# Kernel tuning notes

Hardware: AMD Instinct MI355X
Metric: run time of the kernel (lower is better)

Reference implementation:

```python
import jax, jax.numpy as jnp
import numpy as np

EPS = 1e-8


def setup_inputs() -> dict:
    key = jax.random.key(0)
    k1, k2, k3, k4 = jax.random.split(key, 4)
    N, D, P, H = 8192, 512, 128, 128
    x1 = jax.random.normal(k1, (N, D), dtype=jnp.float32)
    proj_w1 = jax.random.normal(k2, (D, D), dtype=jnp.float32) * (1.0 / np.sqrt(D))
    proj_w2 = jax.random.normal(k3, (D, P), dtype=jnp.float32) * (1.0 / np.sqrt(D))
    gc_w = jax.random.normal(k4, (D, H), dtype=jnp.float32) * (1.0 / np.sqrt(D))
    gc_b = jnp.zeros((H,), dtype=jnp.float32)
    return {"x1": x1, "proj_w1": proj_w1, "proj_w2": proj_w2, "gc_w": gc_w, "gc_b": gc_b}


def _cosine_similarity(x):
    # torch.mm(x, x.T) / clamp(||x|| * ||x||.T, eps)
    w = jnp.sqrt(jnp.sum(x * x, axis=1, keepdims=True))  # [N,1]
    return (x @ x.T) / jnp.maximum(w * w.T, EPS)


def reference(x1, proj_w1, proj_w2, gc_w, gc_b):
    # projector: Linear(512,512,bias=False) -> ReLU -> Linear(512,P,bias=False)
    x_proj = jax.nn.relu(x1 @ proj_w1) @ proj_w2  # [N,P]
    # graph build is under @torch.no_grad(): dense fully-connected weighted graph
    A = jax.lax.stop_gradient(_cosine_similarity(x_proj))  # [N,N]
    N = x1.shape[0]
    # WGraphConv (DGL GraphConv w/ edge weights, norm='both'):
    # fully connected graph incl. self loops -> in_degree = N, norm = N^{-1/2} on both sides
    inv_n = jnp.asarray(1.0 / N, dtype=x1.dtype)
    h = x1 @ gc_w            # project first (D > H, cheaper)  [N,H]
    h = (A @ h) * inv_n      # weighted aggregate, symmetric degree norm
    return h + gc_b          # [N,H]
```

## Files before the change

### kernel.cpp

```cpp
#include <hip/hip_runtime.h>
#include <stdint.h>
#include <stddef.h>

typedef short s16x4 __attribute__((ext_vector_type(4)));
typedef short s16x8 __attribute__((ext_vector_type(8)));
typedef float f32x4 __attribute__((ext_vector_type(4)));

#define NN 8192
#define DD 512
#define PP 128
#define HH 128

__device__ __forceinline__ short f2bf(float f) {
  unsigned u = __builtin_bit_cast(unsigned, f);
  u = (u + 0x7fffu + ((u >> 16) & 1u)) >> 16;
  return (short)u;
}

__device__ __forceinline__ void async16(const void* g, void* l) {
  __builtin_amdgcn_global_load_lds(
      (const __attribute__((address_space(1))) unsigned int*)g,
      (__attribute__((address_space(3))) unsigned int*)l, 16, 0, 0);
}

template <int MF>
__device__ __forceinline__ void gemm_core2(
    const short* __restrict__ A, long lda,
    const short* __restrict__ BT, long ldb,
    long rowBase, long colBase, int k0, int k1,
    short* As0, short* Bs0, short* As1, short* Bs1,
    f32x4 (*acc)[4]) {
  const int tid  = threadIdx.x;
  const int lane = tid & 63;
  const int wid  = tid >> 6;
  const int wr   = (wid >> 1) * (MF * 16);
  const int wc   = (wid & 1) * 64;
  const int srow = lane >> 3;
  const int skk  = (lane & 7) * 8;

#define STAGE_(AS, BS, KK)                                                    \
  do {                                                                        \
    _Pragma("unroll")                                                         \
    for (int it = 0; it < MF; ++it) {                                         \
      int r = wid * (MF * 8) + it * 8;                                        \
      async16(A + (rowBase + r + srow) * lda + (KK) + skk, (AS) + r * 64);    \
    }                                                                         \
    _Pragma("unroll")                                                         \
    for (int it = 0; it < 4; ++it) {                                          \
      int r = wid * 32 + it * 8;                                              \
      async16(BT + (colBase + r + srow) * ldb + (KK) + skk, (BS) + r * 64);   \
    }                                                                         \
  } while (0)

  STAGE_(As0, Bs0, k0);
  __syncthreads();
  for (int k = k0; k < k1; k += 64) {
    if (k + 64 < k1) STAGE_(As1, Bs1, k + 64);
#pragma unroll
    for (int ks = 0; ks < 64; ks += 32) {
      s16x8 af[MF], bfv[4];
#pragma unroll
      for (int i = 0; i < MF; ++i)
        af[i]  = *(const s16x8*)(As0 + (wr + i * 16 + (lane & 15)) * 64 + ks + (lane >> 4) * 8);
#pragma unroll
      for (int i = 0; i < 4; ++i)
        bfv[i] = *(const s16x8*)(Bs0 + (wc + i * 16 + (lane & 15)) * 64 + ks + (lane >> 4) * 8);
#pragma unroll
      for (int mi = 0; mi < MF; ++mi)
#pragma unroll
        for (int ni = 0; ni < 4; ++ni)
          acc[mi][ni] = __builtin_amdgcn_mfma_f32_16x16x32_bf16(af[mi], bfv[ni], acc[mi][ni], 0, 0, 0);
    }
    __syncthreads();
    short* t0 = As0; As0 = As1; As1 = t0;
    short* t1 = Bs0; Bs0 = Bs1; Bs1 = t1;
  }
#undef STAGE_
}

__device__ __forceinline__ void zero_acc2(f32x4 (*acc)[4], int mf) {
  f32x4 z = {0.f, 0.f, 0.f, 0.f};
  for (int i = 0; i < mf; ++i)
    for (int j = 0; j < 4; ++j) acc[i][j] = z;
}

__global__ __launch_bounds__(256) void k_prep(
    const float* __restrict__ x1, const float* __restrict__ w1,
    const float* __restrict__ w2, const float* __restrict__ gcw,
    short* __restrict__ x1b, short* __restrict__ w1t,
    short* __restrict__ w2t, short* __restrict__ gcwt) {
  long b = blockIdx.x;
  int t = threadIdx.x;
  if (b < 4096) {
    long i = b * 256 + t;
    float4 v = ((const float4*)x1)[i];
    s16x4 o;
    o[0] = f2bf(v.x); o[1] = f2bf(v.y); o[2] = f2bf(v.z); o[3] = f2bf(v.w);
    *(s16x4*)(x1b + i * 4) = o;
  } else if (b < 4096 + 1024) {
    long i = (b - 4096) * 256 + t;
    int n = (int)(i >> 9), k = (int)(i & 511);
    w1t[i] = f2bf(w1[(long)k * DD + n]);
  } else if (b < 4096 + 1024 + 256) {
    long i = (b - 5120) * 256 + t;
    int n = (int)(i >> 9), k = (int)(i & 511);
    w2t[i] = f2bf(w2[(long)k * PP + n]);
  } else {
    long i = (b - 5376) * 256 + t;
    int n = (int)(i >> 9), k = (int)(i & 511);
    gcwt[i] = f2bf(gcw[(long)k * HH + n]);
  }
}

__global__ __launch_bounds__(256) void k_g13(const short* __restrict__ x1b,
                                             const short* __restrict__ w1t,
                                             const short* __restrict__ gcwt,
                                             short* __restrict__ Y,
                                             short* __restrict__ hT) {
  __shared__ __align__(16) char smem[49152];
  short* As0 = (short*)smem;
  short* As1 = (short*)(smem + 8192);
  short* Bs0 = (short*)(smem + 16384);
  short* Bs1 = (short*)(smem + 32768);
  f32x4 acc[2][4];
  zero_acc2(acc, 2);
  const int bx = blockIdx.x;
  const int lane = threadIdx.x & 63, wid = threadIdx.x >> 6;
  const int wr = (wid >> 1) * 32, wc = (wid & 1) * 64;
  if (bx < 512) {
    long rowBase = (long)(bx >> 2) * 64;
    long colBase = (long)(bx & 3) * 128;
    gemm_core2<2>(x1b, DD, w1t, DD, rowBase, colBase, 0, DD, As0, Bs0, As1, Bs1, acc);
#pragma unroll
    for (int mi = 0; mi < 2; ++mi)
#pragma unroll
      for (int ni = 0; ni < 4; ++ni)
#pragma unroll
        for (int r = 0; r < 4; ++r) {
          long m = rowBase + wr + mi * 16 + ((lane >> 4) << 2) + r;
          long n = colBase + wc + ni * 16 + (lane & 15);
          float v = acc[mi][ni][r];
          Y[m * DD + n] = f2bf(v > 0.f ? v : 0.f);
        }
  } else {
    long rowBase = (long)(bx - 512) * 64;
    gemm_core2<2>(x1b, DD, gcwt, DD, rowBase, 0, 0, DD, As0, Bs0, As1, Bs1, acc);
    short (*hs)[66] = (short(*)[66])smem;
#pragma unroll
    for (int mi = 0; mi < 2; ++mi)
#pragma unroll
      for (int ni = 0; ni < 4; ++ni)
#pragma unroll
        for (int r = 0; r < 4; ++r) {
          int m = wr + mi * 16 + ((lane >> 4) << 2) + r;
          int n = wc + ni * 16 + (lane & 15);
          hs[n][m] = f2bf(acc[mi][ni][r]);
        }
    __syncthreads();
    int t = threadIdx.x;
    int h = t >> 1, m0 = (t & 1) * 32;
#pragma unroll
    for (int j0 = 0; j0 < 32; j0 += 8) {
      s16x8 o;
#pragma unroll
      for (int u = 0; u < 8; ++u) o[u] = hs[h][m0 + j0 + u];
      *(s16x8*)(hT + (long)h * NN + rowBase + m0 + j0) = o;
    }
  }
}

__global__ __launch_bounds__(256) void k_g2e(const short* __restrict__ Y,
                                             const short* __restrict__ w2t,
                                             const short* __restrict__ hT,
                                             short* __restrict__ xp,
                                             float* __restrict__ invnw,
                                             float* __restrict__ Gp) {
  __shared__ __align__(16) char smem[50176];
  short* As0 = (short*)smem;
  short* As1 = (short*)(smem + 8192);
  short* Bs0 = (short*)(smem + 16384);
  short* Bs1 = (short*)(smem + 32768);
  f32x4 acc[2][4];
  zero_acc2(acc, 2);
  const long rowBase = (long)blockIdx.x * 64;
  gemm_core2<2>(Y, DD, w2t, DD, rowBase, 0, 0, DD, As0, Bs0, As1, Bs1, acc);
  const int t = threadIdx.x;
  const int lane = t & 63, wid = t >> 6;
  {
    const int wr = (wid >> 1) * 32, wc = (wid & 1) * 64;
    float (*xs)[129] = (float(*)[129])smem;
    float* invw_s = (float*)(smem + 49920);
    short* xpt_s = (short*)(smem + 33536);
#pragma unroll
    for (int mi = 0; mi < 2; ++mi)
#pragma unroll
      for (int ni = 0; ni < 4; ++ni)
#pragma unroll
        for (int r = 0; r < 4; ++r)
          xs[wr + mi * 16 + ((lane >> 4) << 2) + r][wc + ni * 16 + (lane & 15)] = acc[mi][ni][r];
    __syncthreads();
    if (t < 64) {
      float s = 0.f;
#pragma unroll 8
      for (int i = 0; i < 128; ++i) { int c = (t + i) & 127; float v = xs[t][c]; s += v * v; }
      float nr = sqrtf(s);
      invnw[rowBase + t] = 1.f / (8192.f * nr);
      invw_s[t] = 1.f / nr;
    }
    __syncthreads();
#pragma unroll
    for (int i = 0; i < 4; ++i) {
      int seg = i * 256 + t;
      int r = seg >> 4, c0 = (seg & 15) * 8;
      s16x8 o;
#pragma unroll
      for (int u = 0; u < 8; ++u) o[u] = f2bf(xs[r][c0 + u]);
      *(s16x8*)(xp + (long)(rowBase + r) * PP + c0) = o;
    }
    int c = t >> 1, n0 = (t & 1) * 32;
#pragma unroll
    for (int j0 = 0; j0 < 32; j0 += 8) {
      s16x8 o;
#pragma unroll
      for (int u = 0; u < 8; ++u) {
        int n = n0 + j0 + u;
        o[u] = f2bf(xs[n][c] * invw_s[n]);
      }
      *(s16x8*)(xpt_s + c * 64 + n0 + j0) = o;
    }
  }
  __syncthreads();
  {
    short* hts = (short*)smem;
    const int srow = lane >> 3, skk = (lane & 7) * 8;
#pragma unroll
    for (int it = 0; it < 4; ++it) {
      int r = wid * 32 + it * 8;
      async16(hT + (long)(r + srow) * NN + rowBase + skk, hts + r * 64);
    }
  }
  __syncthreads();
  {
    const short* xpt_s = (const short*)(smem + 33536);
    const short* hts = (const short*)smem;
    const int wr = (wid >> 1) * 64, wc = (wid & 1) * 64;
    f32x4 acc2[4][4];
    zero_acc2(acc2, 4);
#pragma unroll
    for (int ks = 0; ks < 64; ks += 32) {
      s16x8 af[4], bfv[4];
#pragma unroll
      for (int i = 0; i < 4; ++i)
        af[i]  = *(const s16x8*)(xpt_s + (wr + i * 16 + (lane & 15)) * 64 + ks + (lane >> 4) * 8);
#pragma unroll
      for (int i = 0; i < 4; ++i)
        bfv[i] = *(const s16x8*)(hts + (wc + i * 16 + (lane & 15)) * 64 + ks + (lane >> 4) * 8);
#pragma unroll
      for (int mi = 0; mi < 4; ++mi)
#pragma unroll
        for (int ni = 0; ni < 4; ++ni)
          acc2[mi][ni] = __builtin_amdgcn_mfma_f32_16x16x32_bf16(af[mi], bfv[ni], acc2[mi][ni], 0, 0, 0);
    }
    float* gp = Gp + (long)blockIdx.x * (PP * HH);
#pragma unroll
    for (int mi = 0; mi < 4; ++mi)
#pragma unroll
      for (int ni = 0; ni < 4; ++ni)
#pragma unroll
        for (int r = 0; r < 4; ++r) {
          int m = wr + mi * 16 + ((lane >> 4) << 2) + r;
          int n = wc + ni * 16 + (lane & 15);
          gp[m * HH + n] = acc2[mi][ni][r];
        }
  }
}

__global__ __launch_bounds__(256) void k_red(const float* __restrict__ Gp,
                                             short* __restrict__ GT) {
  int i = blockIdx.x * 256 + threadIdx.x;
  float s = 0.f;
#pragma unroll 8
  for (int j = 0; j < 128; ++j) s += Gp[j * (PP * HH) + i];
  int p = i >> 7, h = i & 127;
  GT[h * PP + p] = f2bf(s);
}

__global__ __launch_bounds__(256) void k_gf(const short* __restrict__ xp,
                                            const short* __restrict__ GT,
                                            const float* __restrict__ invnw,
                                            const float* __restrict__ gcb,
                                            float* __restrict__ out) {
  __shared__ __align__(16) char smem[49152];
  short* As0 = (short*)smem;
  short* As1 = (short*)(smem + 8192);
  short* Bs0 = (short*)(smem + 16384);
  short* Bs1 = (short*)(smem + 32768);
  f32x4 acc[2][4];
  zero_acc2(acc, 2);
  long rowBase = (long)blockIdx.x * 64;
  gemm_core2<2>(xp, PP, GT, PP, rowBase, 0, 0, PP, As0, Bs0, As1, Bs1, acc);
  const int lane = threadIdx.x & 63, wid = threadIdx.x >> 6;
  const int wr = (wid >> 1) * 32, wc = (wid & 1) * 64;
#pragma unroll
  for (int mi = 0; mi < 2; ++mi)
#pragma unroll
    for (int ni = 0; ni < 4; ++ni)
#pragma unroll
      for (int r = 0; r < 4; ++r) {
        long m = rowBase + wr + mi * 16 + ((lane >> 4) << 2) + r;
        int n = wc + ni * 16 + (lane & 15);
        out[m * HH + n] = acc[mi][ni][r] * invnw[m] + gcb[n];
      }
}

extern "C" void kernel_launch(void* const* d_in, const int* in_sizes, int n_in,
                              void* d_out, int out_size, void* d_ws, size_t ws_size,
                              hipStream_t stream) {
  const float* x1  = (const float*)d_in[0];
  const float* w1  = (const float*)d_in[1];
  const float* w2  = (const float*)d_in[2];
  const float* gcw = (const float*)d_in[3];
  const float* gcb = (const float*)d_in[4];
  float* out = (float*)d_out;

  char* ws = (char*)d_ws;
  size_t off = 0;
  auto alloc = [&](size_t bytes) -> char* {
    char* p = ws + off;
    off += (bytes + 255) & ~(size_t)255;
    return p;
  };
  short* x1b  = (short*)alloc((size_t)NN * DD * 2);
  short* w1t  = (short*)alloc((size_t)DD * DD * 2);
  short* w2t  = (short*)alloc((size_t)PP * DD * 2);
  short* gcwt = (short*)alloc((size_t)HH * DD * 2);
  short* Y    = (short*)alloc((size_t)NN * DD * 2);
  short* xp   = (short*)alloc((size_t)NN * PP * 2);
  short* hT   = (short*)alloc((size_t)NN * HH * 2);
  float* invnw = (float*)alloc((size_t)NN * 4);
  float* Gp   = (float*)alloc((size_t)128 * PP * HH * 4);
  short* GT   = (short*)alloc((size_t)PP * HH * 2);

  hipLaunchKernelGGL(k_prep, dim3(5632), dim3(256), 0, stream,
                     x1, w1, w2, gcw, x1b, w1t, w2t, gcwt);
  hipLaunchKernelGGL(k_g13, dim3(640), dim3(256), 0, stream, x1b, w1t, gcwt, Y, hT);
  hipLaunchKernelGGL(k_g2e, dim3(128), dim3(256), 0, stream, Y, w2t, hT, xp, invnw, Gp);
  hipLaunchKernelGGL(k_red, dim3(64), dim3(256), 0, stream, Gp, GT);
  hipLaunchKernelGGL(k_gf, dim3(128), dim3(256), 0, stream, xp, GT, invnw, gcb, out);
}
```

Baseline: 49.94 us.

## Fuse tail kernels into one persistent kernel with atomic grid barriers

Merges the projection/partial-Gram kernel, the reduction kernel and the final GEMM kernel into a single 128-block kernel separated by software grid barriers built on atomic counters. The aim is to remove two kernel launch boundaries and their drain/ramp gaps on a small tail workload. A memset of the counters is added each call. The barrier relies on all 128 blocks being co-resident, and during the reduction only half the threads work.

```diff
diff --git a/kernel.cpp b/kernel.cpp
--- a/kernel.cpp
+++ b/kernel.cpp
@@ -21,6 +21,17 @@
   __builtin_amdgcn_global_load_lds(
       (const __attribute__((address_space(1))) unsigned int*)g,
       (__attribute__((address_space(3))) unsigned int*)l, 16, 0, 0);
+}
+
+__device__ __forceinline__ void gridbar(unsigned* cnt, unsigned expected) {
+  __threadfence();
+  __syncthreads();
+  if (threadIdx.x == 0) {
+    atomicAdd(cnt, 1u);
+    while (atomicAdd(cnt, 0u) < expected) __builtin_amdgcn_s_sleep(2);
+  }
+  __syncthreads();
+  __threadfence();
 }
 
 template <int MF>
@@ -169,148 +180,151 @@
   }
 }
 
-__global__ __launch_bounds__(256) void k_g2e(const short* __restrict__ Y,
-                                             const short* __restrict__ w2t,
-                                             const short* __restrict__ hT,
-                                             short* __restrict__ xp,
-                                             float* __restrict__ invnw,
-                                             float* __restrict__ Gp) {
+__global__ __launch_bounds__(256) void k_tail(const short* __restrict__ Y,
+                                              const short* __restrict__ w2t,
+                                              const short* __restrict__ hT,
+                                              const float* __restrict__ gcb,
+                                              short* __restrict__ xp,
+                                              float* __restrict__ invnw,
+                                              float* __restrict__ Gp,
+                                              short* __restrict__ GT,
+                                              float* __restrict__ out,
+                                              unsigned* __restrict__ cnt) {
   __shared__ __align__(16) char smem[50176];
-  short* As0 = (short*)smem;
-  short* As1 = (short*)(smem + 8192);
-  short* Bs0 = (short*)(smem + 16384);
-  short* Bs1 = (short*)(smem + 32768);
-  f32x4 acc[2][4];
-  zero_acc2(acc, 2);
-  const long rowBase = (long)blockIdx.x * 64;
-  gemm_core2<2>(Y, DD, w2t, DD, rowBase, 0, 0, DD, As0, Bs0, As1, Bs1, acc);
   const int t = threadIdx.x;
   const int lane = t & 63, wid = t >> 6;
+  const long rowBase = (long)blockIdx.x * 64;
+
   {
+    short* As0 = (short*)smem;
+    short* As1 = (short*)(smem + 8192);
+    short* Bs0 = (short*)(smem + 16384);
+    short* Bs1 = (short*)(smem + 32768);
+    f32x4 acc[2][4];
+    zero_acc2(acc, 2);
+    gemm_core2<2>(Y, DD, w2t, DD, rowBase, 0, 0, DD, As0, Bs0, As1, Bs1, acc);
+    {
+      const int wr = (wid >> 1) * 32, wc = (wid & 1) * 64;
+      float (*xs)[129] = (float(*)[129])smem;
+      float* invw_s = (float*)(smem + 49920);
+      short* xpt_s = (short*)(smem + 33536);
+#pragma unroll
+      for (int mi = 0; mi < 2; ++mi)
+#pragma unroll
+        for (int ni = 0; ni < 4; ++ni)
+#pragma unroll
+          for (int r = 0; r < 4; ++r)
+            xs[wr + mi * 16 + ((lane >> 4) << 2) + r][wc + ni * 16 + (lane & 15)] = acc[mi][ni][r];
+      __syncthreads();
+      if (t < 64) {
+        float s = 0.f;
+#pragma unroll 8
+        for (int i = 0; i < 128; ++i) { int c = (t + i) & 127; float v = xs[t][c]; s += v * v; }
+        float nr = sqrtf(s);
+        invnw[rowBase + t] = 1.f / (8192.f * nr);
+        invw_s[t] = 1.f / nr;
+      }
+      __syncthreads();
+#pragma unroll
+      for (int i = 0; i < 4; ++i) {
+        int seg = i * 256 + t;
+        int r = seg >> 4, c0 = (seg & 15) * 8;
+        s16x8 o;
+#pragma unroll
+        for (int u = 0; u < 8; ++u) o[u] = f2bf(xs[r][c0 + u]);
+        *(s16x8*)(xp + (long)(rowBase + r) * PP + c0) = o;
+      }
+      int c = t >> 1, n0 = (t & 1) * 32;
+#pragma unroll
+      for (int j0 = 0; j0 < 32; j0 += 8) {
+        s16x8 o;
+#pragma unroll
+        for (int u = 0; u < 8; ++u) {
+          int n = n0 + j0 + u;
+          o[u] = f2bf(xs[n][c] * invw_s[n]);
+        }
+        *(s16x8*)(xpt_s + c * 64 + n0 + j0) = o;
+      }
+    }
+    __syncthreads();
+    {
+      short* hts = (short*)smem;
+      const int srow = lane >> 3, skk = (lane & 7) * 8;
+#pragma unroll
+      for (int it = 0; it < 4; ++it) {
+        int r = wid * 32 + it * 8;
+        async16(hT + (long)(r + srow) * NN + rowBase + skk, hts + r * 64);
+      }
+    }
+    __syncthreads();
+    {
+      const short* xpt_s = (const short*)(smem + 33536);
+      const short* hts = (const short*)smem;
+      const int wr = (wid >> 1) * 64, wc = (wid & 1) * 64;
+      f32x4 acc2[4][4];
+      zero_acc2(acc2, 4);
+#pragma unroll
+      for (int ks = 0; ks < 64; ks += 32) {
+        s16x8 af[4], bfv[4];
+#pragma unroll
+        for (int i = 0; i < 4; ++i)
+          af[i]  = *(const s16x8*)(xpt_s + (wr + i * 16 + (lane & 15)) * 64 + ks + (lane >> 4) * 8);
+#pragma unroll
+        for (int i = 0; i < 4; ++i)
+          bfv[i] = *(const s16x8*)(hts + (wc + i * 16 + (lane & 15)) * 64 + ks + (lane >> 4) * 8);
+#pragma unroll
+        for (int mi = 0; mi < 4; ++mi)
+#pragma unroll
+          for (int ni = 0; ni < 4; ++ni)
+            acc2[mi][ni] = __builtin_amdgcn_mfma_f32_16x16x32_bf16(af[mi], bfv[ni], acc2[mi][ni], 0, 0, 0);
+      }
+      float* gp = Gp + (long)blockIdx.x * (PP * HH);
+#pragma unroll
+      for (int mi = 0; mi < 4; ++mi)
+#pragma unroll
+        for (int ni = 0; ni < 4; ++ni)
+#pragma unroll
+          for (int r = 0; r < 4; ++r) {
+            int m = wr + mi * 16 + ((lane >> 4) << 2) + r;
+            int n = wc + ni * 16 + (lane & 15);
+            gp[m * HH + n] = acc2[mi][ni][r];
+          }
+    }
+  }
+
+  gridbar(cnt, 128);
+
+  if (t < 128) {
+    int i = blockIdx.x * 128 + t;
+    float s = 0.f;
+#pragma unroll 8
+    for (int j = 0; j < 128; ++j) s += Gp[j * (PP * HH) + i];
+    int p = i >> 7, h = i & 127;
+    GT[h * PP + p] = f2bf(s);
+  }
+
+  gridbar(cnt + 1, 128);
+
+  {
+    short* As0 = (short*)smem;
+    short* As1 = (short*)(smem + 8192);
+    short* Bs0 = (short*)(smem + 16384);
+    short* Bs1 = (short*)(smem + 32768);
+    f32x4 acc[2][4];
+    zero_acc2(acc, 2);
+    gemm_core2<2>(xp, PP, GT, PP, rowBase, 0, 0, PP, As0, Bs0, As1, Bs1, acc);
     const int wr = (wid >> 1) * 32, wc = (wid & 1) * 64;
-    float (*xs)[129] = (float(*)[129])smem;
-    float* invw_s = (float*)(smem + 49920);
-    short* xpt_s = (short*)(smem + 33536);
 #pragma unroll
     for (int mi = 0; mi < 2; ++mi)
 #pragma unroll
       for (int ni = 0; ni < 4; ++ni)
 #pragma unroll
-        for (int r = 0; r < 4; ++r)
-          xs[wr + mi * 16 + ((lane >> 4) << 2) + r][wc + ni * 16 + (lane & 15)] = acc[mi][ni][r];
-    __syncthreads();
-    if (t < 64) {
-      float s = 0.f;
-#pragma unroll 8
-      for (int i = 0; i < 128; ++i) { int c = (t + i) & 127; float v = xs[t][c]; s += v * v; }
-      float nr = sqrtf(s);
-      invnw[rowBase + t] = 1.f / (8192.f * nr);
-      invw_s[t] = 1.f / nr;
-    }
-    __syncthreads();
-#pragma unroll
-    for (int i = 0; i < 4; ++i) {
-      int seg = i * 256 + t;
-      int r = seg >> 4, c0 = (seg & 15) * 8;
-      s16x8 o;
-#pragma unroll
-      for (int u = 0; u < 8; ++u) o[u] = f2bf(xs[r][c0 + u]);
-      *(s16x8*)(xp + (long)(rowBase + r) * PP + c0) = o;
-    }
-    int c = t >> 1, n0 = (t & 1) * 32;
-#pragma unroll
-    for (int j0 = 0; j0 < 32; j0 += 8) {
-      s16x8 o;
-#pragma unroll
-      for (int u = 0; u < 8; ++u) {
-        int n = n0 + j0 + u;
-        o[u] = f2bf(xs[n][c] * invw_s[n]);
-      }
-      *(s16x8*)(xpt_s + c * 64 + n0 + j0) = o;
-    }
-  }
-  __syncthreads();
-  {
-    short* hts = (short*)smem;
-    const int srow = lane >> 3, skk = (lane & 7) * 8;
-#pragma unroll
-    for (int it = 0; it < 4; ++it) {
-      int r = wid * 32 + it * 8;
-      async16(hT + (long)(r + srow) * NN + rowBase + skk, hts + r * 64);
-    }
-  }
-  __syncthreads();
-  {
-    const short* xpt_s = (const short*)(smem + 33536);
-    const short* hts = (const short*)smem;
-    const int wr = (wid >> 1) * 64, wc = (wid & 1) * 64;
-    f32x4 acc2[4][4];
-    zero_acc2(acc2, 4);
-#pragma unroll
-    for (int ks = 0; ks < 64; ks += 32) {
-      s16x8 af[4], bfv[4];
-#pragma unroll
-      for (int i = 0; i < 4; ++i)
-        af[i]  = *(const s16x8*)(xpt_s + (wr + i * 16 + (lane & 15)) * 64 + ks + (lane >> 4) * 8);
-#pragma unroll
-      for (int i = 0; i < 4; ++i)
-        bfv[i] = *(const s16x8*)(hts + (wc + i * 16 + (lane & 15)) * 64 + ks + (lane >> 4) * 8);
-#pragma unroll
-      for (int mi = 0; mi < 4; ++mi)
-#pragma unroll
-        for (int ni = 0; ni < 4; ++ni)
-          acc2[mi][ni] = __builtin_amdgcn_mfma_f32_16x16x32_bf16(af[mi], bfv[ni], acc2[mi][ni], 0, 0, 0);
-    }
-    float* gp = Gp + (long)blockIdx.x * (PP * HH);
-#pragma unroll
-    for (int mi = 0; mi < 4; ++mi)
-#pragma unroll
-      for (int ni = 0; ni < 4; ++ni)
-#pragma unroll
         for (int r = 0; r < 4; ++r) {
-          int m = wr + mi * 16 + ((lane >> 4) << 2) + r;
+          long m = rowBase + wr + mi * 16 + ((lane >> 4) << 2) + r;
           int n = wc + ni * 16 + (lane & 15);
-          gp[m * HH + n] = acc2[mi][ni][r];
+          out[m * HH + n] = acc[mi][ni][r] * invnw[m] + gcb[n];
         }
   }
-}
-
-__global__ __launch_bounds__(256) void k_red(const float* __restrict__ Gp,
-                                             short* __restrict__ GT) {
-  int i = blockIdx.x * 256 + threadIdx.x;
-  float s = 0.f;
-#pragma unroll 8
-  for (int j = 0; j < 128; ++j) s += Gp[j * (PP * HH) + i];
-  int p = i >> 7, h = i & 127;
-  GT[h * PP + p] = f2bf(s);
-}
-
-__global__ __launch_bounds__(256) void k_gf(const short* __restrict__ xp,
-                                            const short* __restrict__ GT,
-                                            const float* __restrict__ invnw,
-                                            const float* __restrict__ gcb,
-                                            float* __restrict__ out) {
-  __shared__ __align__(16) char smem[49152];
-  short* As0 = (short*)smem;
-  short* As1 = (short*)(smem + 8192);
-  short* Bs0 = (short*)(smem + 16384);
-  short* Bs1 = (short*)(smem + 32768);
-  f32x4 acc[2][4];
-  zero_acc2(acc, 2);
-  long rowBase = (long)blockIdx.x * 64;
-  gemm_core2<2>(xp, PP, GT, PP, rowBase, 0, 0, PP, As0, Bs0, As1, Bs1, acc);
-  const int lane = threadIdx.x & 63, wid = threadIdx.x >> 6;
-  const int wr = (wid >> 1) * 32, wc = (wid & 1) * 64;
-#pragma unroll
-  for (int mi = 0; mi < 2; ++mi)
-#pragma unroll
-    for (int ni = 0; ni < 4; ++ni)
-#pragma unroll
-      for (int r = 0; r < 4; ++r) {
-        long m = rowBase + wr + mi * 16 + ((lane >> 4) << 2) + r;
-        int n = wc + ni * 16 + (lane & 15);
-        out[m * HH + n] = acc[mi][ni][r] * invnw[m] + gcb[n];
-      }
 }
 
 extern "C" void kernel_launch(void* const* d_in, const int* in_sizes, int n_in,
@@ -340,11 +354,12 @@
   float* invnw = (float*)alloc((size_t)NN * 4);
   float* Gp   = (float*)alloc((size_t)128 * PP * HH * 4);
   short* GT   = (short*)alloc((size_t)PP * HH * 2);
-
+  unsigned* cnt = (unsigned*)alloc(256);
+
+  hipMemsetAsync(cnt, 0, 8, stream);
   hipLaunchKernelGGL(k_prep, dim3(5632), dim3(256), 0, stream,
                      x1, w1, w2, gcw, x1b, w1t, w2t, gcwt);
   hipLaunchKernelGGL(k_g13, dim3(640), dim3(256), 0, stream, x1b, w1t, gcwt, Y, hT);
-  hipLaunchKernelGGL(k_g2e, dim3(128), dim3(256), 0, stream, Y, w2t, hT, xp, invnw, Gp);
-  hipLaunchKernelGGL(k_red, dim3(64), dim3(256), 0, stream, Gp, GT);
-  hipLaunchKernelGGL(k_gf, dim3(128), dim3(256), 0, stream, xp, GT, invnw, gcb, out);
-}
+  hipLaunchKernelGGL(k_tail, dim3(128), dim3(256), 0, stream,
+                     Y, w2t, hT, gcb, xp, invnw, Gp, GT, out, cnt);
+}
```

After: 101.3 us. 103% more time.

## Fuse x1 bf16 conversion into first GEMM and tile-transpose weight prep

Applied to the files above, without the earlier changes.

Removes the separate pass that converted x1 (16 MB fp32) to a bf16 copy. The first GEMM kernel now loads fp32 x1 directly into registers, converts it, and writes bf16 into LDS, with software prefetch of the next k-tile. Weight transposes now go through an LDS tile with coalesced reads and writes, and that kernel runs only 96 blocks. The cost is that x1 is reread as fp32 by every column block of the GEMM (4 for G1 plus 1 for the gc GEMM), which adds global traffic and register pressure.

```diff
diff --git a/kernel.cpp b/kernel.cpp
--- a/kernel.cpp
+++ b/kernel.cpp
@@ -84,35 +84,37 @@
     for (int j = 0; j < 4; ++j) acc[i][j] = z;
 }
 
-__global__ __launch_bounds__(256) void k_prep(
-    const float* __restrict__ x1, const float* __restrict__ w1,
-    const float* __restrict__ w2, const float* __restrict__ gcw,
-    short* __restrict__ x1b, short* __restrict__ w1t,
-    short* __restrict__ w2t, short* __restrict__ gcwt) {
-  long b = blockIdx.x;
-  int t = threadIdx.x;
-  if (b < 4096) {
-    long i = b * 256 + t;
-    float4 v = ((const float4*)x1)[i];
+__global__ __launch_bounds__(256) void k_prep_w(
+    const float* __restrict__ w1, const float* __restrict__ w2,
+    const float* __restrict__ gcw,
+    short* __restrict__ w1t, short* __restrict__ w2t, short* __restrict__ gcwt) {
+  __shared__ float tile[64][65];
+  int b = blockIdx.x, t = threadIdx.x;
+  const float* src; short* dst; int K0, N0, ldn;
+  if (b < 64)      { src = w1;  dst = w1t;  ldn = 512; K0 = (b >> 3) * 64;        N0 = (b & 7) * 64; }
+  else if (b < 80) { int bb = b - 64; src = w2;  dst = w2t;  ldn = 128; K0 = (bb >> 1) * 64; N0 = (bb & 1) * 64; }
+  else             { int bb = b - 80; src = gcw; dst = gcwt; ldn = 128; K0 = (bb >> 1) * 64; N0 = (bb & 1) * 64; }
+#pragma unroll
+  for (int i = 0; i < 4; ++i) {
+    int idx = i * 1024 + t * 4;
+    int row = idx >> 6, col = idx & 63;
+    float4 v = *(const float4*)(src + (long)(K0 + row) * ldn + N0 + col);
+    tile[row][col] = v.x; tile[row][col + 1] = v.y;
+    tile[row][col + 2] = v.z; tile[row][col + 3] = v.w;
+  }
+  __syncthreads();
+#pragma unroll
+  for (int i = 0; i < 4; ++i) {
+    int idx = i * 1024 + t * 4;
+    int n = idx >> 6, k = idx & 63;
     s16x4 o;
-    o[0] = f2bf(v.x); o[1] = f2bf(v.y); o[2] = f2bf(v.z); o[3] = f2bf(v.w);
-    *(s16x4*)(x1b + i * 4) = o;
-  } else if (b < 4096 + 1024) {
-    long i = (b - 4096) * 256 + t;
-    int n = (int)(i >> 9), k = (int)(i & 511);
-    w1t[i] = f2bf(w1[(long)k * DD + n]);
-  } else if (b < 4096 + 1024 + 256) {
-    long i = (b - 5120) * 256 + t;
-    int n = (int)(i >> 9), k = (int)(i & 511);
-    w2t[i] = f2bf(w2[(long)k * PP + n]);
-  } else {
-    long i = (b - 5376) * 256 + t;
-    int n = (int)(i >> 9), k = (int)(i & 511);
-    gcwt[i] = f2bf(gcw[(long)k * HH + n]);
-  }
-}
-
-__global__ __launch_bounds__(256) void k_g13(const short* __restrict__ x1b,
+#pragma unroll
+    for (int u = 0; u < 4; ++u) o[u] = f2bf(tile[k + u][n]);
+    *(s16x4*)(dst + (long)(N0 + n) * DD + K0 + k) = o;
+  }
+}
+
+__global__ __launch_bounds__(256) void k_g13(const float* __restrict__ x1,
                                              const short* __restrict__ w1t,
                                              const short* __restrict__ gcwt,
                                              short* __restrict__ Y,
@@ -124,13 +126,67 @@
   short* Bs1 = (short*)(smem + 32768);
   f32x4 acc[2][4];
   zero_acc2(acc, 2);
+  const int tid = threadIdx.x;
+  const int lane = tid & 63, wid = tid >> 6;
+  const int wr = (wid >> 1) * 32, wc = (wid & 1) * 64;
+  const int srow = lane >> 3, skk = (lane & 7) * 8;
+  const int arow = tid >> 2, ac0 = (tid & 3) * 16;
   const int bx = blockIdx.x;
-  const int lane = threadIdx.x & 63, wid = threadIdx.x >> 6;
-  const int wr = (wid >> 1) * 32, wc = (wid & 1) * 64;
-  if (bx < 512) {
-    long rowBase = (long)(bx >> 2) * 64;
-    long colBase = (long)(bx & 3) * 128;
-    gemm_core2<2>(x1b, DD, w1t, DD, rowBase, colBase, 0, DD, As0, Bs0, As1, Bs1, acc);
+  const bool isG1 = bx < 512;
+  const long rowBase = isG1 ? (long)(bx >> 2) * 64 : (long)(bx - 512) * 64;
+  const long colBase = isG1 ? (long)(bx & 3) * 128 : 0;
+  const short* BT = isG1 ? w1t : gcwt;
+  const float* aptr = x1 + (rowBase + arow) * DD + ac0;
+
+  float4 a0, a1, a2, a3;
+#define LOADA_(KK)                                                            \
+  do { const float4* p = (const float4*)(aptr + (KK));                        \
+       a0 = p[0]; a1 = p[1]; a2 = p[2]; a3 = p[3]; } while (0)
+#define LOADB_(BS, KK)                                                        \
+  do { _Pragma("unroll")                                                      \
+    for (int it = 0; it < 4; ++it) {                                          \
+      int r = wid * 32 + it * 8;                                              \
+      async16(BT + (colBase + r + srow) * DD + (KK) + skk, (BS) + r * 64);    \
+    } } while (0)
+#define WRITEA_(AS)                                                           \
+  do { s16x8 o0, o1;                                                          \
+    o0[0]=f2bf(a0.x); o0[1]=f2bf(a0.y); o0[2]=f2bf(a0.z); o0[3]=f2bf(a0.w);   \
+    o0[4]=f2bf(a1.x); o0[5]=f2bf(a1.y); o0[6]=f2bf(a1.z); o0[7]=f2bf(a1.w);   \
+    o1[0]=f2bf(a2.x); o1[1]=f2bf(a2.y); o1[2]=f2bf(a2.z); o1[3]=f2bf(a2.w);   \
+    o1[4]=f2bf(a3.x); o1[5]=f2bf(a3.y); o1[6]=f2bf(a3.z); o1[7]=f2bf(a3.w);   \
+    *(s16x8*)((AS) + arow * 64 + ac0)     = o0;                               \
+    *(s16x8*)((AS) + arow * 64 + ac0 + 8) = o1; } while (0)
+
+  LOADA_(0); LOADB_(Bs0, 0); WRITEA_(As0);
+  __syncthreads();
+  for (int k = 0; k < DD; k += 64) {
+    const bool more = (k + 64 < DD);
+    if (more) { LOADA_(k + 64); LOADB_(Bs1, k + 64); }
+#pragma unroll
+    for (int ks = 0; ks < 64; ks += 32) {
+      s16x8 af[2], bfv[4];
+#pragma unroll
+      for (int i = 0; i < 2; ++i)
+        af[i]  = *(const s16x8*)(As0 + (wr + i * 16 + (lane & 15)) * 64 + ks + (lane >> 4) * 8);
+#pragma unroll
+      for (int i = 0; i < 4; ++i)
+        bfv[i] = *(const s16x8*)(Bs0 + (wc + i * 16 + (lane & 15)) * 64 + ks + (lane >> 4) * 8);
+#pragma unroll
+      for (int mi = 0; mi < 2; ++mi)
+#pragma unroll
+        for (int ni = 0; ni < 4; ++ni)
+          acc[mi][ni] = __builtin_amdgcn_mfma_f32_16x16x32_bf16(af[mi], bfv[ni], acc[mi][ni], 0, 0, 0);
+    }
+    if (more) WRITEA_(As1);
+    __syncthreads();
+    short* t0 = As0; As0 = As1; As1 = t0;
+    short* t1 = Bs0; Bs0 = Bs1; Bs1 = t1;
+  }
+#undef LOADA_
+#undef LOADB_
+#undef WRITEA_
+
+  if (isG1) {
 #pragma unroll
     for (int mi = 0; mi < 2; ++mi)
 #pragma unroll
@@ -143,8 +199,6 @@
           Y[m * DD + n] = f2bf(v > 0.f ? v : 0.f);
         }
   } else {
-    long rowBase = (long)(bx - 512) * 64;
-    gemm_core2<2>(x1b, DD, gcwt, DD, rowBase, 0, 0, DD, As0, Bs0, As1, Bs1, acc);
     short (*hs)[66] = (short(*)[66])smem;
 #pragma unroll
     for (int mi = 0; mi < 2; ++mi)
@@ -157,8 +211,7 @@
           hs[n][m] = f2bf(acc[mi][ni][r]);
         }
     __syncthreads();
-    int t = threadIdx.x;
-    int h = t >> 1, m0 = (t & 1) * 32;
+    int h = tid >> 1, m0 = (tid & 1) * 32;
 #pragma unroll
     for (int j0 = 0; j0 < 32; j0 += 8) {
       s16x8 o;
@@ -330,7 +383,6 @@
     off += (bytes + 255) & ~(size_t)255;
     return p;
   };
-  short* x1b  = (short*)alloc((size_t)NN * DD * 2);
   short* w1t  = (short*)alloc((size_t)DD * DD * 2);
   short* w2t  = (short*)alloc((size_t)PP * DD * 2);
   short* gcwt = (short*)alloc((size_t)HH * DD * 2);
@@ -341,9 +393,8 @@
   float* Gp   = (float*)alloc((size_t)128 * PP * HH * 4);
   short* GT   = (short*)alloc((size_t)PP * HH * 2);
 
-  hipLaunchKernelGGL(k_prep, dim3(5632), dim3(256), 0, stream,
-                     x1, w1, w2, gcw, x1b, w1t, w2t, gcwt);
-  hipLaunchKernelGGL(k_g13, dim3(640), dim3(256), 0, stream, x1b, w1t, gcwt, Y, hT);
+  hipLaunchKernelGGL(k_prep_w, dim3(96), dim3(256), 0, stream, w1, w2, gcw, w1t, w2t, gcwt);
+  hipLaunchKernelGGL(k_g13, dim3(640), dim3(256), 0, stream, x1, w1t, gcwt, Y, hT);
   hipLaunchKernelGGL(k_g2e, dim3(128), dim3(256), 0, stream, Y, w2t, hT, xp, invnw, Gp);
   hipLaunchKernelGGL(k_red, dim3(64), dim3(256), 0, stream, Gp, GT);
   hipLaunchKernelGGL(k_gf, dim3(128), dim3(256), 0, stream, xp, GT, invnw, gcb, out);
```

Result: slower. 53.56 us (+7.2%).

## Halve row tiles in tail GEMMs and use LDS-tiled weight transposes

Applied to the files above, without the earlier changes.

The weight transpose-and-convert step now goes through a 64x64 shared-memory tile, so global reads and writes are coalesced instead of strided per-element. The projection/epilogue kernel and the final GEMM now process 32 rows per block instead of 64, doubling grid size to 256 blocks to fill more of the GPU's compute units. The partial Gram reduction sums 256 partials instead of 128. In exchange, per-block reuse drops and the reduction kernel reads twice as much partial data.

```diff
diff --git a/kernel.cpp b/kernel.cpp
--- a/kernel.cpp
+++ b/kernel.cpp
@@ -89,6 +89,7 @@
     const float* __restrict__ w2, const float* __restrict__ gcw,
     short* __restrict__ x1b, short* __restrict__ w1t,
     short* __restrict__ w2t, short* __restrict__ gcwt) {
+  __shared__ float tile[64][65];
   long b = blockIdx.x;
   int t = threadIdx.x;
   if (b < 4096) {
@@ -97,18 +98,30 @@
     s16x4 o;
     o[0] = f2bf(v.x); o[1] = f2bf(v.y); o[2] = f2bf(v.z); o[3] = f2bf(v.w);
     *(s16x4*)(x1b + i * 4) = o;
-  } else if (b < 4096 + 1024) {
-    long i = (b - 4096) * 256 + t;
-    int n = (int)(i >> 9), k = (int)(i & 511);
-    w1t[i] = f2bf(w1[(long)k * DD + n]);
-  } else if (b < 4096 + 1024 + 256) {
-    long i = (b - 5120) * 256 + t;
-    int n = (int)(i >> 9), k = (int)(i & 511);
-    w2t[i] = f2bf(w2[(long)k * PP + n]);
-  } else {
-    long i = (b - 5376) * 256 + t;
-    int n = (int)(i >> 9), k = (int)(i & 511);
-    gcwt[i] = f2bf(gcw[(long)k * HH + n]);
+    return;
+  }
+  int bb = (int)(b - 4096);
+  const float* src; short* dst; int K0, N0, ldn;
+  if (bb < 64)      { src = w1;  dst = w1t;  ldn = 512; K0 = (bb >> 3) * 64; N0 = (bb & 7) * 64; }
+  else if (bb < 80) { int c = bb - 64; src = w2;  dst = w2t;  ldn = 128; K0 = (c >> 1) * 64; N0 = (c & 1) * 64; }
+  else              { int c = bb - 80; src = gcw; dst = gcwt; ldn = 128; K0 = (c >> 1) * 64; N0 = (c & 1) * 64; }
+#pragma unroll
+  for (int i = 0; i < 4; ++i) {
+    int idx = i * 1024 + t * 4;
+    int row = idx >> 6, col = idx & 63;
+    float4 v = *(const float4*)(src + (long)(K0 + row) * ldn + N0 + col);
+    tile[row][col] = v.x; tile[row][col + 1] = v.y;
+    tile[row][col + 2] = v.z; tile[row][col + 3] = v.w;
+  }
+  __syncthreads();
+#pragma unroll
+  for (int i = 0; i < 4; ++i) {
+    int idx = i * 1024 + t * 4;
+    int n = idx >> 6, k = idx & 63;
+    s16x4 o;
+#pragma unroll
+    for (int u = 0; u < 4; ++u) o[u] = f2bf(tile[k + u][n]);
+    *(s16x4*)(dst + (long)(N0 + n) * DD + K0 + k) = o;
   }
 }
 
@@ -175,31 +188,29 @@
                                              short* __restrict__ xp,
                                              float* __restrict__ invnw,
                                              float* __restrict__ Gp) {
-  __shared__ __align__(16) char smem[50176];
+  __shared__ __align__(16) char smem[41216];
   short* As0 = (short*)smem;
-  short* As1 = (short*)(smem + 8192);
-  short* Bs0 = (short*)(smem + 16384);
-  short* Bs1 = (short*)(smem + 32768);
-  f32x4 acc[2][4];
-  zero_acc2(acc, 2);
-  const long rowBase = (long)blockIdx.x * 64;
-  gemm_core2<2>(Y, DD, w2t, DD, rowBase, 0, 0, DD, As0, Bs0, As1, Bs1, acc);
+  short* As1 = (short*)(smem + 4096);
+  short* Bs0 = (short*)(smem + 8192);
+  short* Bs1 = (short*)(smem + 24576);
+  f32x4 acc[1][4];
+  zero_acc2(acc, 1);
+  const long rowBase = (long)blockIdx.x * 32;
+  gemm_core2<1>(Y, DD, w2t, DD, rowBase, 0, 0, DD, As0, Bs0, As1, Bs1, acc);
   const int t = threadIdx.x;
   const int lane = t & 63, wid = t >> 6;
   {
-    const int wr = (wid >> 1) * 32, wc = (wid & 1) * 64;
+    const int wr = (wid >> 1) * 16, wc = (wid & 1) * 64;
     float (*xs)[129] = (float(*)[129])smem;
-    float* invw_s = (float*)(smem + 49920);
-    short* xpt_s = (short*)(smem + 33536);
-#pragma unroll
-    for (int mi = 0; mi < 2; ++mi)
-#pragma unroll
-      for (int ni = 0; ni < 4; ++ni)
-#pragma unroll
-        for (int r = 0; r < 4; ++r)
-          xs[wr + mi * 16 + ((lane >> 4) << 2) + r][wc + ni * 16 + (lane & 15)] = acc[mi][ni][r];
+    short* xpt_s = (short*)(smem + 16640);
+    float* invw_s = (float*)(smem + 40960);
+#pragma unroll
+    for (int ni = 0; ni < 4; ++ni)
+#pragma unroll
+      for (int r = 0; r < 4; ++r)
+        xs[wr + ((lane >> 4) << 2) + r][wc + ni * 16 + (lane & 15)] = acc[0][ni][r];
     __syncthreads();
-    if (t < 64) {
+    if (t < 32) {
       float s = 0.f;
 #pragma unroll 8
       for (int i = 0; i < 128; ++i) { int c = (t + i) & 127; float v = xs[t][c]; s += v * v; }
@@ -209,7 +220,7 @@
     }
     __syncthreads();
 #pragma unroll
-    for (int i = 0; i < 4; ++i) {
+    for (int i = 0; i < 2; ++i) {
       int seg = i * 256 + t;
       int r = seg >> 4, c0 = (seg & 15) * 8;
       s16x8 o;
@@ -217,50 +228,46 @@
       for (int u = 0; u < 8; ++u) o[u] = f2bf(xs[r][c0 + u]);
       *(s16x8*)(xp + (long)(rowBase + r) * PP + c0) = o;
     }
-    int c = t >> 1, n0 = (t & 1) * 32;
-#pragma unroll
-    for (int j0 = 0; j0 < 32; j0 += 8) {
+    int c = t >> 1, n0 = (t & 1) * 16;
+#pragma unroll
+    for (int j0 = 0; j0 < 16; j0 += 8) {
       s16x8 o;
 #pragma unroll
       for (int u = 0; u < 8; ++u) {
         int n = n0 + j0 + u;
         o[u] = f2bf(xs[n][c] * invw_s[n]);
       }
-      *(s16x8*)(xpt_s + c * 64 + n0 + j0) = o;
+      *(s16x8*)(xpt_s + c * 32 + n0 + j0) = o;
     }
   }
   __syncthreads();
   {
-    short* hts = (short*)smem;
-    const int srow = lane >> 3, skk = (lane & 7) * 8;
-#pragma unroll
-    for (int it = 0; it < 4; ++it) {
-      int r = wid * 32 + it * 8;
-      async16(hT + (long)(r + srow) * NN + rowBase + skk, hts + r * 64);
+    short* hts = (short*)(smem + 32768);
+#pragma unroll
+    for (int it = 0; it < 2; ++it) {
+      int r = wid * 32 + it * 16;
+      async16(hT + (long)(r + (lane >> 2)) * NN + rowBase + (lane & 3) * 8, hts + r * 32);
     }
   }
   __syncthreads();
   {
-    const short* xpt_s = (const short*)(smem + 33536);
-    const short* hts = (const short*)smem;
+    const short* xpt_s = (const short*)(smem + 16640);
+    const short* hts = (const short*)(smem + 32768);
     const int wr = (wid >> 1) * 64, wc = (wid & 1) * 64;
     f32x4 acc2[4][4];
     zero_acc2(acc2, 4);
-#pragma unroll
-    for (int ks = 0; ks < 64; ks += 32) {
-      s16x8 af[4], bfv[4];
-#pragma unroll
-      for (int i = 0; i < 4; ++i)
-        af[i]  = *(const s16x8*)(xpt_s + (wr + i * 16 + (lane & 15)) * 64 + ks + (lane >> 4) * 8);
-#pragma unroll
-      for (int i = 0; i < 4; ++i)
-        bfv[i] = *(const s16x8*)(hts + (wc + i * 16 + (lane & 15)) * 64 + ks + (lane >> 4) * 8);
-#pragma unroll
-      for (int mi = 0; mi < 4; ++mi)
-#pragma unroll
-        for (int ni = 0; ni < 4; ++ni)
-          acc2[mi][ni] = __builtin_amdgcn_mfma_f32_16x16x32_bf16(af[mi], bfv[ni], acc2[mi][ni], 0, 0, 0);
-    }
+    s16x8 af[4], bfv[4];
+#pragma unroll
+    for (int i = 0; i < 4; ++i)
+      af[i]  = *(const s16x8*)(xpt_s + (wr + i * 16 + (lane & 15)) * 32 + (lane >> 4) * 8);
+#pragma unroll
+    for (int i = 0; i < 4; ++i)
+      bfv[i] = *(const s16x8*)(hts + (wc + i * 16 + (lane & 15)) * 32 + (lane >> 4) * 8);
+#pragma unroll
+    for (int mi = 0; mi < 4; ++mi)
+#pragma unroll
+      for (int ni = 0; ni < 4; ++ni)
+        acc2[mi][ni] = __builtin_amdgcn_mfma_f32_16x16x32_bf16(af[mi], bfv[ni], acc2[mi][ni], 0, 0, 0);
     float* gp = Gp + (long)blockIdx.x * (PP * HH);
 #pragma unroll
     for (int mi = 0; mi < 4; ++mi)
@@ -275,12 +282,12 @@
   }
 }
 
-__global__ __launch_bounds__(256) void k_red(const float* __restrict__ Gp,
+__global__ __launch_bounds__(128) void k_red(const float* __restrict__ Gp,
                                              short* __restrict__ GT) {
-  int i = blockIdx.x * 256 + threadIdx.x;
+  int i = blockIdx.x * 128 + threadIdx.x;
   float s = 0.f;
 #pragma unroll 8
-  for (int j = 0; j < 128; ++j) s += Gp[j * (PP * HH) + i];
+  for (int j = 0; j < 256; ++j) s += Gp[j * (PP * HH) + i];
   int p = i >> 7, h = i & 127;
   GT[h * PP + p] = f2bf(s);
 }
@@ -290,27 +297,25 @@
                                             const float* __restrict__ invnw,
                                             const float* __restrict__ gcb,
                                             float* __restrict__ out) {
-  __shared__ __align__(16) char smem[49152];
+  __shared__ __align__(16) char smem[40960];
   short* As0 = (short*)smem;
-  short* As1 = (short*)(smem + 8192);
-  short* Bs0 = (short*)(smem + 16384);
-  short* Bs1 = (short*)(smem + 32768);
-  f32x4 acc[2][4];
-  zero_acc2(acc, 2);
-  long rowBase = (long)blockIdx.x * 64;
-  gemm_core2<2>(xp, PP, GT, PP, rowBase, 0, 0, PP, As0, Bs0, As1, Bs1, acc);
+  short* As1 = (short*)(smem + 4096);
+  short* Bs0 = (short*)(smem + 8192);
+  short* Bs1 = (short*)(smem + 24576);
+  f32x4 acc[1][4];
+  zero_acc2(acc, 1);
+  long rowBase = (long)blockIdx.x * 32;
+  gemm_core2<1>(xp, PP, GT, PP, rowBase, 0, 0, PP, As0, Bs0, As1, Bs1, acc);
   const int lane = threadIdx.x & 63, wid = threadIdx.x >> 6;
-  const int wr = (wid >> 1) * 32, wc = (wid & 1) * 64;
-#pragma unroll
-  for (int mi = 0; mi < 2; ++mi)
-#pragma unroll
-    for (int ni = 0; ni < 4; ++ni)
-#pragma unroll
-      for (int r = 0; r < 4; ++r) {
-        long m = rowBase + wr + mi * 16 + ((lane >> 4) << 2) + r;
-        int n = wc + ni * 16 + (lane & 15);
-        out[m * HH + n] = acc[mi][ni][r] * invnw[m] + gcb[n];
-      }
+  const int wr = (wid >> 1) * 16, wc = (wid & 1) * 64;
+#pragma unroll
+  for (int ni = 0; ni < 4; ++ni)
+#pragma unroll
+    for (int r = 0; r < 4; ++r) {
+      long m = rowBase + wr + ((lane >> 4) << 2) + r;
+      int n = wc + ni * 16 + (lane & 15);
+      out[m * HH + n] = acc[0][ni][r] * invnw[m] + gcb[n];
+    }
 }
 
 extern "C" void kernel_launch(void* const* d_in, const int* in_sizes, int n_in,
@@ -338,13 +343,13 @@
   short* xp   = (short*)alloc((size_t)NN * PP * 2);
   short* hT   = (short*)alloc((size_t)NN * HH * 2);
   float* invnw = (float*)alloc((size_t)NN * 4);
-  float* Gp   = (float*)alloc((size_t)128 * PP * HH * 4);
+  float* Gp   = (float*)alloc((size_t)256 * PP * HH * 4);
   short* GT   = (short*)alloc((size_t)PP * HH * 2);
 
-  hipLaunchKernelGGL(k_prep, dim3(5632), dim3(256), 0, stream,
+  hipLaunchKernelGGL(k_prep, dim3(4192), dim3(256), 0, stream,
                      x1, w1, w2, gcw, x1b, w1t, w2t, gcwt);
   hipLaunchKernelGGL(k_g13, dim3(640), dim3(256), 0, stream, x1b, w1t, gcwt, Y, hT);
-  hipLaunchKernelGGL(k_g2e, dim3(128), dim3(256), 0, stream, Y, w2t, hT, xp, invnw, Gp);
-  hipLaunchKernelGGL(k_red, dim3(64), dim3(256), 0, stream, Gp, GT);
-  hipLaunchKernelGGL(k_gf, dim3(128), dim3(256), 0, stream, xp, GT, invnw, gcb, out);
-}
+  hipLaunchKernelGGL(k_g2e, dim3(256), dim3(256), 0, stream, Y, w2t, hT, xp, invnw, Gp);
+  hipLaunchKernelGGL(k_red, dim3(128), dim3(128), 0, stream, Gp, GT);
+  hipLaunchKernelGGL(k_gf, dim3(256), dim3(256), 0, stream, xp, GT, invnw, gcb, out);
+}
```

New measurement: 53.00 us. 6.1% more time.
